# Kernel optimization log

Hardware: AMD Instinct MI355X
Metric: run time of the kernel (lower is better)

The kernel has to match this reference:

```python
import math
import jax, jax.numpy as jnp
import numpy as np

B, T_BI, D_BI = 64, 3000, 128
T_SW, D_SW = 375, 192
T_S1, D_S1 = 188, 192
N_FIRES = 300          # static fire count (target_lengths all = 300 -> beta = 1, ceil(sum)=300)
D_MODEL = 512
SCALE = 4.0            # scale_factor
EPS_LN = 1e-5


def _cif_integrate(h, alpha, thr, n_fires):
    """Vectorized CIF: cumsum + two scatter-adds (matches torch _cif_forward).
    h [B,T,D], alpha [B,T], thr [B,1] -> [B,n_fires,D]."""
    Bq, T, D = h.shape
    a = alpha / thr                       # normalize so boundaries sit at integers
    c = jnp.cumsum(a, axis=1)
    prev = c - a
    kp = jnp.floor(prev)
    kc = jnp.floor(c)
    fired = kc > kp                       # frame crosses a token boundary
    w_hi = jnp.where(fired, (c - kc) * thr, 0.0)          # leftover into new token
    w_lo = jnp.where(fired, (kp + 1.0 - prev) * thr, alpha)  # portion completing old token
    ip = jnp.clip(kp.astype(jnp.int32), 0, n_fires - 1)
    ic = jnp.clip(kc.astype(jnp.int32), 0, n_fires - 1)
    bidx = jnp.broadcast_to(jnp.arange(Bq)[:, None], (Bq, T))
    out = jnp.zeros((Bq, n_fires, D), h.dtype)
    out = out.at[bidx, ip].add(w_lo[..., None] * h)
    out = out.at[bidx, ic].add(w_hi[..., None] * h)
    return out


def _interp(src, t_cont, t_bi):
    """Linear interp of src [B,Ts,D] at continuous fire times t_cont [B,N] (given on the T_bi grid)."""
    Bq, Ts, D = src.shape
    t = t_cont * Ts / t_bi
    lo = jnp.clip(t.astype(jnp.int32), 0, Ts - 2)
    w = (t - lo.astype(t.dtype))[..., None]
    idx_lo = jnp.broadcast_to(lo[..., None], (Bq, t.shape[1], D))
    g_lo = jnp.take_along_axis(src, idx_lo, axis=1)
    g_hi = jnp.take_along_axis(src, idx_lo + 1, axis=1)
    return (1.0 - w) * g_lo + w * g_hi


def _forward(fire_signal, acoustic_src, acoustic_src_s1, conv_w, ln_g, ln_b, wp_w, wp_b,
             film_s0_w, film_s0_b, film_s1_w, film_s1_b, tproj_w, tproj_b,
             aproj_w, aproj_b, bproj_w, bproj_b, target_lengths):
    Bq, T_bi, _ = fire_signal.shape
    # 1) weight predictor: depthwise conv (k=1, no bias) -> LN -> Linear -> sigmoid
    x = fire_signal * conv_w                                   # depthwise 1x1 conv
    mu = jnp.mean(x, axis=-1, keepdims=True)
    var = jnp.var(x, axis=-1, keepdims=True)
    xn = (x - mu) * jax.lax.rsqrt(var + EPS_LN) * ln_g + ln_b
    alpha = SCALE * jax.nn.sigmoid(xn @ wp_w + wp_b)           # [B,T]
    tgt = target_lengths.astype(alpha.dtype)
    qty_loss = jnp.mean(jnp.abs(jnp.sum(alpha, axis=1) - tgt))
    # training-mode alpha normalization (sum alpha_cif == target)
    sum_a = jnp.clip(jnp.sum(alpha, axis=1, keepdims=True), 1e-8)
    alpha_cif = alpha * (tgt[:, None] / sum_a)
    # dynamic threshold beta = sum / ceil(sum)  (== 1 here since targets are integers)
    sum_cif = jnp.sum(alpha_cif, axis=1)
    ceil_sum = jax.lax.stop_gradient(jnp.clip(jnp.ceil(sum_cif), 1.0))
    thr = (sum_cif / ceil_sum)[:, None]                        # [B,1]
    # 2) CIF integration of temporal channel
    acoustic_temporal = _cif_integrate(fire_signal, alpha_cif, thr, N_FIRES)  # [B,N,128]
    # continuous fire times
    cum = jnp.cumsum(alpha_cif, axis=1)
    thresholds = jnp.arange(1, N_FIRES + 1, dtype=alpha.dtype)[None, :] * thr  # [B,N]
    ff = jax.vmap(jnp.searchsorted)(cum, thresholds)
    ff = jnp.minimum(ff, T_bi - 1)
    t_lo = jnp.maximum(ff - 1, 0)
    cum_at = jnp.take_along_axis(cum, t_lo, axis=1)
    a_at = jnp.take_along_axis(alpha_cif, ff, axis=1)
    t_cont = t_lo.astype(alpha.dtype) + (thresholds - cum_at) / jnp.clip(a_at, 1e-8)
    t_cont = jnp.clip(t_cont, 0.0, T_bi - 1)
    # 3) S0 pitch channel: interp + FiLM
    acoustic_pitch = _interp(acoustic_src, t_cont, T_bi)       # [B,N,192]
    film0 = acoustic_temporal @ film_s0_w + film_s0_b
    g0, b0 = jnp.split(film0, 2, axis=-1)
    pitch_mod = g0 * acoustic_pitch + b0
    # 4) project + combine
    embs = (acoustic_temporal @ tproj_w + tproj_b) + (pitch_mod @ aproj_w + aproj_b)
    # S1 beat channel
    acoustic_beat = _interp(acoustic_src_s1, t_cont, T_bi)     # [B,N,192]
    film1 = acoustic_temporal @ film_s1_w + film_s1_b
    g1, b1 = jnp.split(film1, 2, axis=-1)
    beat_mod = g1 * acoustic_beat + b1
    embs = embs + (beat_mod @ bproj_w + bproj_b)
    return embs, alpha, qty_loss


def setup_inputs() -> dict:
    key = jax.random.key(0)
    ks = jax.random.split(key, 14)
    # weight_proj bias init per module: alpha_init = target_fires/encoder_len
    p = min((128.0 / 3000.0) / SCALE, 0.99)
    wp_bias = math.log(p / (1.0 - p))
    f32 = jnp.float32
    return {
        "fire_signal": jax.random.normal(ks[0], (B, T_BI, D_BI), f32),
        "acoustic_src": jax.random.normal(ks[1], (B, T_SW, D_SW), f32),
        "acoustic_src_s1": jax.random.normal(ks[2], (B, T_S1, D_S1), f32),
        "target_lengths": jnp.full((B,), N_FIRES, jnp.int32),
        "conv_w": 1.0 + 0.1 * jax.random.normal(ks[3], (D_BI,), f32),
        "ln_g": jnp.ones((D_BI,), f32),
        "ln_b": jnp.zeros((D_BI,), f32),
        "wp_w": 0.02 * jax.random.normal(ks[4], (D_BI,), f32),
        "wp_b": jnp.asarray(wp_bias, f32),
        "film_s0_w": 0.02 * jax.random.normal(ks[5], (D_BI, 2 * D_SW), f32),
        "film_s0_b": jnp.concatenate([jnp.ones((D_SW,), f32), jnp.zeros((D_SW,), f32)]),
        "film_s1_w": 0.02 * jax.random.normal(ks[6], (D_BI, 2 * D_S1), f32),
        "film_s1_b": jnp.concatenate([jnp.ones((D_S1,), f32), jnp.zeros((D_S1,), f32)]),
        "tproj_w": 0.02 * jax.random.normal(ks[7], (D_BI, D_MODEL), f32),
        "tproj_b": jnp.zeros((D_MODEL,), f32),
        "aproj_w": 0.02 * jax.random.normal(ks[8], (D_SW, D_MODEL), f32),
        "aproj_b": jnp.zeros((D_MODEL,), f32),
        "bproj_w": 0.02 * jax.random.normal(ks[9], (D_S1, D_MODEL), f32),
        "bproj_b": jnp.zeros((D_MODEL,), f32),
    }


def reference(fire_signal, acoustic_src, acoustic_src_s1, target_lengths, conv_w, ln_g, ln_b,
              wp_w, wp_b, film_s0_w, film_s0_b, film_s1_w, film_s1_b, tproj_w, tproj_b,
              aproj_w, aproj_b, bproj_w, bproj_b):
    return _forward(fire_signal, acoustic_src, acoustic_src_s1, conv_w, ln_g, ln_b, wp_w, wp_b,
                    film_s0_w, film_s0_b, film_s1_w, film_s1_b, tproj_w, tproj_b,
                    aproj_w, aproj_b, bproj_w, bproj_b, target_lengths)
```

## Files before the change

kernel.cpp:

```cpp
#include <hip/hip_runtime.h>
#include <math.h>

#define BQ 64
#define TBI 3000
#define DBI 128
#define TSW 375
#define TS1 188
#define DSW 192
#define NF 300
#define DMODEL 512
#define EPSLN 1e-5f

typedef __bf16 bf16x8 __attribute__((ext_vector_type(8)));
typedef float f32x4 __attribute__((ext_vector_type(4)));

__device__ __forceinline__ unsigned short f2bf(float f) {
    unsigned u = __float_as_uint(f);
    unsigned r = (u + 0x7FFFu + ((u >> 16) & 1u)) >> 16;
    return (unsigned short)r;
}

#define ALPHA_BLOCKS 24000

__global__ __launch_bounds__(256) void k_alpha_prep(
    const float* __restrict__ fs, const float* __restrict__ conv_w,
    const float* __restrict__ ln_g, const float* __restrict__ ln_b,
    const float* __restrict__ wp_w, const float* __restrict__ wp_b,
    float* __restrict__ alpha_out,
    const float* __restrict__ f0w, const float* __restrict__ f1w,
    const float* __restrict__ tw, const float* __restrict__ aw, const float* __restrict__ bw,
    const float* __restrict__ f0b, const float* __restrict__ f1b,
    const float* __restrict__ tb, const float* __restrict__ apb, const float* __restrict__ bpb,
    unsigned short* __restrict__ Wg, unsigned short* __restrict__ Wb,
    unsigned short* __restrict__ W2,
    float* __restrict__ gbias, float* __restrict__ bbias, float* __restrict__ bias2,
    float* __restrict__ qtyo)
{
    if (blockIdx.x >= ALPHA_BLOCKS) {
        int pbid = blockIdx.x - ALPHA_BLOCKS;
        if (pbid == 1216) {
            for (int c = threadIdx.x; c < 512; c += 256) {
                if (c < 384) {
                    gbias[c] = c < 192 ? f0b[c] : f1b[c - 192];
                    bbias[c] = c < 192 ? f0b[c + 192] : f1b[c - 192 + 192];
                }
                bias2[c] = tb[c] + apb[c] + bpb[c];
            }
            if (threadIdx.x == 0) qtyo[0] = 0.f;
            return;
        }
        int i = pbid * 256 + threadIdx.x;
        if (i < 49152) {
            int j = i & 7, lane = (i >> 3) & 63, kt = (i >> 9) & 3, nt = i >> 11;
            int k = kt * 32 + (lane >> 4) * 8 + j;
            int n = nt * 16 + (lane & 15);
            float g, b;
            if (n < 192) { g = f0w[k * 384 + n];         b = f0w[k * 384 + n + 192]; }
            else         { g = f1w[k * 384 + (n - 192)]; b = f1w[k * 384 + (n - 192) + 192]; }
            Wg[i] = f2bf(g); Wb[i] = f2bf(b);
        } else {
            int ii = i - 49152;
            int j = ii & 7, lane = (ii >> 3) & 63, kt = (ii >> 9) & 15, nt = ii >> 13;
            int k = kt * 32 + (lane >> 4) * 8 + j;
            int n = nt * 16 + (lane & 15);
            float v;
            if (k < 128)      v = tw[k * 512 + n];
            else if (k < 320) v = aw[(k - 128) * 512 + n];
            else              v = bw[(k - 320) * 512 + n];
            W2[ii] = f2bf(v);
        }
        return;
    }
    int wave = threadIdx.x >> 6, lane = threadIdx.x & 63;
    int l = lane & 31;
    long g = (long)blockIdx.x * 8 + wave * 2 + (lane >> 5);
    const float* row = fs + g * DBI;
    float4 f  = *(const float4*)&row[4 * l];
    float4 cw = *(const float4*)&conv_w[4 * l];
    float4 x; x.x = f.x * cw.x; x.y = f.y * cw.y; x.z = f.z * cw.z; x.w = f.w * cw.w;
    float s = x.x + x.y + x.z + x.w;
    for (int m = 16; m >= 1; m >>= 1) s += __shfl_xor(s, m, 64);
    float mu = s * (1.0f / 128.0f);
    float4 d; d.x = x.x - mu; d.y = x.y - mu; d.z = x.z - mu; d.w = x.w - mu;
    float q = d.x * d.x + d.y * d.y + d.z * d.z + d.w * d.w;
    for (int m = 16; m >= 1; m >>= 1) q += __shfl_xor(q, m, 64);
    float var = q * (1.0f / 128.0f);
    float rs = rsqrtf(var + EPSLN);
    float4 lg = *(const float4*)&ln_g[4 * l];
    float4 lb = *(const float4*)&ln_b[4 * l];
    float4 wp = *(const float4*)&wp_w[4 * l];
    float z = (d.x * rs * lg.x + lb.x) * wp.x + (d.y * rs * lg.y + lb.y) * wp.y
            + (d.z * rs * lg.z + lb.z) * wp.z + (d.w * rs * lg.w + lb.w) * wp.w;
    for (int m = 16; m >= 1; m >>= 1) z += __shfl_xor(z, m, 64);
    z += wp_b[0];
    float a = 4.0f / (1.0f + expf(-z));
    if (l == 0) alpha_out[g] = a;
}

__global__ __launch_bounds__(1024) void k_scan4(
    const float* __restrict__ alpha, const int* __restrict__ tlen,
    float2* __restrict__ params, float* __restrict__ qtyo,
    float2* __restrict__ c2, float* __restrict__ tcont, int* __restrict__ ffout)
{
    __shared__ float2 sc[TBI];
    __shared__ float2 part[2][1024];
    __shared__ double wpart[16];
    int b = blockIdx.x, tid = threadIdx.x;
    int wv = tid >> 6, ln = tid & 63;
    const float* ar = alpha + (long)b * TBI;
    double s = 0.0;
    for (int t = tid; t < TBI; t += 1024) s += (double)ar[t];
    for (int m = 32; m >= 1; m >>= 1) s += __shfl_xor(s, m, 64);
    if (ln == 0) wpart[wv] = s;
    __syncthreads();
    if (wv == 0) {
        double d = (ln < 16) ? wpart[ln] : 0.0;
        for (int m = 8; m >= 1; m >>= 1) d += __shfl_xor(d, m, 64);
        if (ln == 0) wpart[0] = d;
    }
    __syncthreads();
    double sum_a = wpart[0];
    __syncthreads();
    double tgt = (double)tlen[b];
    double sa = sum_a < 1e-8 ? 1e-8 : sum_a;
    float r = (float)(tgt / sa);
    double s2 = 0.0;
    for (int t = tid; t < TBI; t += 1024) s2 += (double)(ar[t] * r);
    for (int m = 32; m >= 1; m >>= 1) s2 += __shfl_xor(s2, m, 64);
    if (ln == 0) wpart[wv] = s2;
    __syncthreads();
    if (wv == 0) {
        double d = (ln < 16) ? wpart[ln] : 0.0;
        for (int m = 8; m >= 1; m >>= 1) d += __shfl_xor(d, m, 64);
        if (ln == 0) wpart[0] = d;
    }
    __syncthreads();
    float sum_cif = (float)wpart[0];
    float cs = ceilf(sum_cif); if (cs < 1.0f) cs = 1.0f;
    float thr = sum_cif / cs;
    float rthr = 1.0f / thr;
    if (tid == 0) {
        params[b] = make_float2(r, thr);
        atomicAdd(qtyo, (float)fabs(sum_a - tgt) * (1.0f / (float)BQ));
    }
    int base = tid * 3;
    float2 run = make_float2(0.f, 0.f);
    if (base < TBI) {
        for (int j = 0; j < 3; ++j) {
            int t = base + j;
            float ac = ar[t] * r;
            run.x += ac * rthr; run.y += ac;
            sc[t] = run;
        }
    }
    part[0][tid] = (base < TBI) ? run : make_float2(0.f, 0.f);
    __syncthreads();
    int srcb = 0;
    for (int d = 1; d < 1024; d <<= 1) {
        float2 v = part[srcb][tid];
        if (tid >= d) { float2 u = part[srcb][tid - d]; v.x += u.x; v.y += u.y; }
        part[srcb ^ 1][tid] = v;
        srcb ^= 1;
        __syncthreads();
    }
    if (base < TBI && tid > 0) {
        float2 off = part[srcb][tid - 1];
        for (int j = 0; j < 3; ++j) { sc[base + j].x += off.x; sc[base + j].y += off.y; }
    }
    __syncthreads();
    for (int t = tid; t < TBI; t += 1024) {
        float ac = ar[t] * r;
        c2[(long)b * TBI + t] = make_float2(sc[t].x, ac);
    }
    if (tid < NF) {
        float v = (float)(tid + 1) * thr;
        int lo = 0, hi = TBI;
        while (lo < hi) { int mid = (lo + hi) >> 1; if (sc[mid].y < v) lo = mid + 1; else hi = mid; }
        int ff = lo; if (ff > TBI - 1) ff = TBI - 1;
        ffout[b * NF + tid] = ff;
        int tl = ff - 1; if (tl < 0) tl = 0;
        float cum_at = sc[tl].y;
        float a_at = ar[ff] * r;
        if (a_at < 1e-8f) a_at = 1e-8f;
        float tc = (float)tl + (v - cum_at) / a_at;
        tc = fminf(fmaxf(tc, 0.0f), (float)(TBI - 1));
        tcont[b * NF + tid] = tc;
    }
}

__global__ __launch_bounds__(256) void k_cif5(
    const float* __restrict__ fs, const float2* __restrict__ c2,
    const int* __restrict__ ffA, const float2* __restrict__ params,
    unsigned short* __restrict__ at)
{
    int wid = threadIdx.x >> 6, lane = threadIdx.x & 63;
    int wg = blockIdx.x * 4 + wid;
    int b = wg / NF, j = wg - b * NF;
    const int* ffb = ffA + b * NF;
    int s = (j == 0) ? 0 : ffb[j - 1];
    int e = (j == NF - 1) ? (TBI - 1) : ffb[j];
    float thr = params[b].y;
    float rthr = 1.0f / thr;
    const float2* cb = c2 + (long)b * TBI;
    const float* fb = fs + (long)b * TBI * DBI;
    float a0 = 0.f, a1 = 0.f;
    #define CIF_BODY(T) do { \
        float2 v = cb[T]; \
        float2 h = *(const float2*)&fb[(long)(T) * DBI + 2 * lane]; \
        float c = v.x, ac = v.y; \
        float av = ac * rthr; \
        float prev = c - av; \
        float kp = floorf(prev), kc = floorf(c); \
        bool fired = kc > kp; \
        float w_lo = fired ? (kp + 1.0f - prev) * thr : ac; \
        float w_hi = fired ? (c - kc) * thr : 0.0f; \
        int ip = (int)kp; if (ip > NF - 1) ip = NF - 1; if (ip < 0) ip = 0; \
        int ic = (int)kc; if (ic > NF - 1) ic = NF - 1; if (ic < 0) ic = 0; \
        if (ip == j) { a0 += w_lo * h.x; a1 += w_lo * h.y; } \
        if (fired && ic == j) { a0 += w_hi * h.x; a1 += w_hi * h.y; } \
    } while (0)
    int t = s;
    for (; t + 1 <= e; t += 2) { CIF_BODY(t); CIF_BODY(t + 1); }
    if (t <= e) CIF_BODY(t);
    #undef CIF_BODY
    unsigned short* ab = at + (long)b * NF * DBI;
    *(unsigned*)&ab[j * DBI + 2 * lane] = (unsigned)f2bf(a0) | ((unsigned)f2bf(a1) << 16);
}

#define EROWS 32
__global__ __launch_bounds__(512, 4) void k_emb8(
    const unsigned short* __restrict__ atb, const float* __restrict__ tcont,
    const float* __restrict__ src0, const float* __restrict__ src1,
    const unsigned short* __restrict__ Wg, const unsigned short* __restrict__ Wb,
    const unsigned short* __restrict__ W2,
    const float* __restrict__ gbias, const float* __restrict__ bbias,
    const float* __restrict__ bias2, float* __restrict__ embs)
{
    __shared__ __align__(16) unsigned short X[EROWS][520];
    __shared__ float s_w0[EROWS], s_w1[EROWS];
    __shared__ int s_lo0[EROWS], s_lo1[EROWS], s_b[EROWS];
    int tid = threadIdx.x;
    int wave = tid >> 6, lane = tid & 63;
    long r0 = (long)blockIdx.x * EROWS;
    {
        int r = tid >> 4, k8 = (tid & 15) * 8;
        *(uint4*)&X[r][k8] = *(const uint4*)&atb[(r0 + r) * DBI + k8];
    }
    if (tid < EROWS) {
        long g = r0 + tid;
        s_b[tid] = (int)(g / NF);
        float tc = tcont[g];
        float t0 = tc * ((float)TSW / 3000.0f);
        int lo0 = (int)t0; if (lo0 > TSW - 2) lo0 = TSW - 2; if (lo0 < 0) lo0 = 0;
        s_lo0[tid] = lo0; s_w0[tid] = t0 - (float)lo0;
        float t1 = tc * ((float)TS1 / 3000.0f);
        int lo1 = (int)t1; if (lo1 > TS1 - 2) lo1 = TS1 - 2; if (lo1 < 0) lo1 = 0;
        s_lo1[tid] = lo1; s_w1[tid] = t1 - (float)lo1;
    }
    __syncthreads();
    int mrow = lane & 15, quad = lane >> 4;
    float v0[3][2][4], v1[3][2][4], wgt[3][2][4];
    float gbv[3], bbv_[3];
    #pragma unroll
    for (int i = 0; i < 3; ++i) {
        int nt = wave + 8 * i;
        int c = nt * 16 + mrow;
        bool sel = c >= DSW;
        int cc = sel ? c - DSW : c;
        const float* S = sel ? src1 : src0;
        int Ts = sel ? TS1 : TSW;
        gbv[i] = gbias[c]; bbv_[i] = bbias[c];
        #pragma unroll
        for (int m = 0; m < 2; ++m) {
            #pragma unroll
            for (int q = 0; q < 4; ++q) {
                int r = 16 * m + quad * 4 + q;
                int bb = s_b[r];
                int lo = sel ? s_lo1[r] : s_lo0[r];
                float w = sel ? s_w1[r] : s_w0[r];
                const float* Sp = S + ((long)bb * Ts + lo) * DSW + cc;
                v0[i][m][q] = Sp[0];
                v1[i][m][q] = Sp[DSW];
                wgt[i][m][q] = w;
            }
        }
    }
    #pragma unroll
    for (int i = 0; i < 3; ++i) {
        int nt = wave + 8 * i;
        f32x4 ag0 = {0,0,0,0}, ab0 = {0,0,0,0}, ag1 = {0,0,0,0}, ab1 = {0,0,0,0};
        #pragma unroll
        for (int kt = 0; kt < 4; ++kt) {
            bf16x8 a0 = *(const bf16x8*)&X[mrow][kt * 32 + quad * 8];
            bf16x8 a1 = *(const bf16x8*)&X[mrow + 16][kt * 32 + quad * 8];
            bf16x8 bg = *(const bf16x8*)&Wg[(((nt * 4 + kt) * 64) + lane) * 8];
            bf16x8 bb = *(const bf16x8*)&Wb[(((nt * 4 + kt) * 64) + lane) * 8];
            ag0 = __builtin_amdgcn_mfma_f32_16x16x32_bf16(a0, bg, ag0, 0, 0, 0);
            ab0 = __builtin_amdgcn_mfma_f32_16x16x32_bf16(a0, bb, ab0, 0, 0, 0);
            ag1 = __builtin_amdgcn_mfma_f32_16x16x32_bf16(a1, bg, ag1, 0, 0, 0);
            ab1 = __builtin_amdgcn_mfma_f32_16x16x32_bf16(a1, bb, ab1, 0, 0, 0);
        }
        int c = nt * 16 + mrow;
        float gb = gbv[i], bbv = bbv_[i];
        #pragma unroll
        for (int q = 0; q < 4; ++q) {
            {
                int r = quad * 4 + q;
                float w = wgt[i][0][q];
                float pv = (1.0f - w) * v0[i][0][q] + w * v1[i][0][q];
                X[r][128 + c] = f2bf((ag0[q] + gb) * pv + (ab0[q] + bbv));
            }
            {
                int r = quad * 4 + q + 16;
                float w = wgt[i][1][q];
                float pv = (1.0f - w) * v0[i][1][q] + w * v1[i][1][q];
                X[r][128 + c] = f2bf((ag1[q] + gb) * pv + (ab1[q] + bbv));
            }
        }
    }
    __syncthreads();
    f32x4 acc[2][4];
    #pragma unroll
    for (int h = 0; h < 2; ++h)
        #pragma unroll
        for (int n = 0; n < 4; ++n) acc[h][n] = (f32x4){0, 0, 0, 0};
    for (int kt = 0; kt < 16; ++kt) {
        bf16x8 a0 = *(const bf16x8*)&X[mrow][kt * 32 + quad * 8];
        bf16x8 a1 = *(const bf16x8*)&X[mrow + 16][kt * 32 + quad * 8];
        #pragma unroll
        for (int n = 0; n < 4; ++n) {
            int nt = wave * 4 + n;
            bf16x8 bfv = *(const bf16x8*)&W2[((nt * 16 + kt) * 64 + lane) * 8];
            acc[0][n] = __builtin_amdgcn_mfma_f32_16x16x32_bf16(a0, bfv, acc[0][n], 0, 0, 0);
            acc[1][n] = __builtin_amdgcn_mfma_f32_16x16x32_bf16(a1, bfv, acc[1][n], 0, 0, 0);
        }
    }
    #pragma unroll
    for (int n = 0; n < 4; ++n) {
        int cbase = (wave * 4 + n) * 16 + mrow;
        float bv = bias2[cbase];
        #pragma unroll
        for (int q = 0; q < 4; ++q) {
            embs[(r0 + quad * 4 + q) * DMODEL + cbase] = acc[0][n][q] + bv;
            embs[(r0 + 16 + quad * 4 + q) * DMODEL + cbase] = acc[1][n][q] + bv;
        }
    }
}

extern "C" void kernel_launch(void* const* d_in, const int* in_sizes, int n_in,
                              void* d_out, int out_size, void* d_ws, size_t ws_size,
                              hipStream_t stream)
{
    const float* fs     = (const float*)d_in[0];
    const float* src0   = (const float*)d_in[1];
    const float* src1   = (const float*)d_in[2];
    const int*   tlen   = (const int*)d_in[3];
    const float* conv_w = (const float*)d_in[4];
    const float* ln_g   = (const float*)d_in[5];
    const float* ln_b   = (const float*)d_in[6];
    const float* wp_w   = (const float*)d_in[7];
    const float* wp_b   = (const float*)d_in[8];
    const float* f0w    = (const float*)d_in[9];
    const float* f0b    = (const float*)d_in[10];
    const float* f1w    = (const float*)d_in[11];
    const float* f1b    = (const float*)d_in[12];
    const float* tw     = (const float*)d_in[13];
    const float* tb     = (const float*)d_in[14];
    const float* aw     = (const float*)d_in[15];
    const float* apb    = (const float*)d_in[16];
    const float* bw     = (const float*)d_in[17];
    const float* bpb    = (const float*)d_in[18];

    float* embs  = (float*)d_out;
    float* alpha = embs + (long)BQ * NF * DMODEL;
    float* qtyo  = alpha + (long)BQ * TBI;

    char* ws = (char*)d_ws;
    size_t off = 0;
    unsigned short* at = (unsigned short*)(ws + off); off += 4915200;
    float2* c2     = (float2*)(ws + off); off += 1536000;
    float*  tcont  = (float*)(ws + off);  off += 76800;
    int*    ffA    = (int*)(ws + off);    off += 76800;
    float2* params = (float2*)(ws + off); off += 512;
    unsigned short* Wg = (unsigned short*)(ws + off); off += 98304;
    unsigned short* Wb = (unsigned short*)(ws + off); off += 98304;
    unsigned short* W2 = (unsigned short*)(ws + off); off += 524288;
    float* gbias = (float*)(ws + off); off += 1536;
    float* bbias = (float*)(ws + off); off += 1536;
    float* bias2 = (float*)(ws + off); off += 2048;

    k_alpha_prep<<<ALPHA_BLOCKS + 1217, 256, 0, stream>>>(
        fs, conv_w, ln_g, ln_b, wp_w, wp_b, alpha,
        f0w, f1w, tw, aw, bw, f0b, f1b, tb, apb, bpb,
        Wg, Wb, W2, gbias, bbias, bias2, qtyo);
    k_scan4<<<BQ, 1024, 0, stream>>>(alpha, tlen, params, qtyo, c2, tcont, ffA);
    k_cif5<<<(BQ * NF) / 4, 256, 0, stream>>>(fs, c2, ffA, params, at);
    k_emb8<<<(BQ * NF) / EROWS, 512, 0, stream>>>(at, tcont, src0, src1,
                                                  Wg, Wb, W2, gbias, bbias, bias2, embs);
}
```

Before: 264.6 us.

## Halve embedding kernel block size and load interp sources inline after MFMA

The embedding kernel now uses 256 threads (4 waves) per 32-row block instead of 512. Each wave handles twice as many FiLM and output column tiles (6 FiLM tiles, 8 output tiles). The interpolation source values are no longer prefetched into a large register array before the MFMAs; they are loaded inline in the epilogue. This cuts register pressure and raises per-wave W2 reuse of the A fragments, but exposes gather latency after the MFMAs and lowers parallelism per block.

```diff
diff --git a/kernel.cpp b/kernel.cpp
--- a/kernel.cpp
+++ b/kernel.cpp
@@ -228,7 +228,7 @@
 }
 
 #define EROWS 32
-__global__ __launch_bounds__(512, 4) void k_emb8(
+__global__ __launch_bounds__(256, 3) void k_emb9(
     const unsigned short* __restrict__ atb, const float* __restrict__ tcont,
     const float* __restrict__ src0, const float* __restrict__ src1,
     const unsigned short* __restrict__ Wg, const unsigned short* __restrict__ Wb,
@@ -242,8 +242,8 @@
     int tid = threadIdx.x;
     int wave = tid >> 6, lane = tid & 63;
     long r0 = (long)blockIdx.x * EROWS;
-    {
-        int r = tid >> 4, k8 = (tid & 15) * 8;
+    for (int idx = tid; idx < 512; idx += 256) {
+        int r = idx >> 4, k8 = (idx & 15) * 8;
         *(uint4*)&X[r][k8] = *(const uint4*)&atb[(r0 + r) * DBI + k8];
     }
     if (tid < EROWS) {
@@ -259,35 +259,8 @@
     }
     __syncthreads();
     int mrow = lane & 15, quad = lane >> 4;
-    float v0[3][2][4], v1[3][2][4], wgt[3][2][4];
-    float gbv[3], bbv_[3];
-    #pragma unroll
-    for (int i = 0; i < 3; ++i) {
-        int nt = wave + 8 * i;
-        int c = nt * 16 + mrow;
-        bool sel = c >= DSW;
-        int cc = sel ? c - DSW : c;
-        const float* S = sel ? src1 : src0;
-        int Ts = sel ? TS1 : TSW;
-        gbv[i] = gbias[c]; bbv_[i] = bbias[c];
-        #pragma unroll
-        for (int m = 0; m < 2; ++m) {
-            #pragma unroll
-            for (int q = 0; q < 4; ++q) {
-                int r = 16 * m + quad * 4 + q;
-                int bb = s_b[r];
-                int lo = sel ? s_lo1[r] : s_lo0[r];
-                float w = sel ? s_w1[r] : s_w0[r];
-                const float* Sp = S + ((long)bb * Ts + lo) * DSW + cc;
-                v0[i][m][q] = Sp[0];
-                v1[i][m][q] = Sp[DSW];
-                wgt[i][m][q] = w;
-            }
-        }
-    }
-    #pragma unroll
-    for (int i = 0; i < 3; ++i) {
-        int nt = wave + 8 * i;
+    for (int i = 0; i < 6; ++i) {
+        int nt = wave + 4 * i;
         f32x4 ag0 = {0,0,0,0}, ab0 = {0,0,0,0}, ag1 = {0,0,0,0}, ab1 = {0,0,0,0};
         #pragma unroll
         for (int kt = 0; kt < 4; ++kt) {
@@ -301,43 +274,53 @@
             ab1 = __builtin_amdgcn_mfma_f32_16x16x32_bf16(a1, bb, ab1, 0, 0, 0);
         }
         int c = nt * 16 + mrow;
-        float gb = gbv[i], bbv = bbv_[i];
+        bool sel = c >= DSW;
+        int cc = sel ? c - DSW : c;
+        const float* S = sel ? src1 : src0;
+        int Ts = sel ? TS1 : TSW;
+        float gb = gbias[c], bbv = bbias[c];
         #pragma unroll
         for (int q = 0; q < 4; ++q) {
             {
                 int r = quad * 4 + q;
-                float w = wgt[i][0][q];
-                float pv = (1.0f - w) * v0[i][0][q] + w * v1[i][0][q];
+                int b = s_b[r];
+                int lo = sel ? s_lo1[r] : s_lo0[r];
+                float w = sel ? s_w1[r] : s_w0[r];
+                const float* Sp = S + ((long)b * Ts + lo) * DSW + cc;
+                float pv = (1.0f - w) * Sp[0] + w * Sp[DSW];
                 X[r][128 + c] = f2bf((ag0[q] + gb) * pv + (ab0[q] + bbv));
             }
             {
                 int r = quad * 4 + q + 16;
-                float w = wgt[i][1][q];
-                float pv = (1.0f - w) * v0[i][1][q] + w * v1[i][1][q];
+                int b = s_b[r];
+                int lo = sel ? s_lo1[r] : s_lo0[r];
+                float w = sel ? s_w1[r] : s_w0[r];
+                const float* Sp = S + ((long)b * Ts + lo) * DSW + cc;
+                float pv = (1.0f - w) * Sp[0] + w * Sp[DSW];
                 X[r][128 + c] = f2bf((ag1[q] + gb) * pv + (ab1[q] + bbv));
             }
         }
     }
     __syncthreads();
-    f32x4 acc[2][4];
+    f32x4 acc[2][8];
     #pragma unroll
     for (int h = 0; h < 2; ++h)
         #pragma unroll
-        for (int n = 0; n < 4; ++n) acc[h][n] = (f32x4){0, 0, 0, 0};
+        for (int n = 0; n < 8; ++n) acc[h][n] = (f32x4){0, 0, 0, 0};
     for (int kt = 0; kt < 16; ++kt) {
         bf16x8 a0 = *(const bf16x8*)&X[mrow][kt * 32 + quad * 8];
         bf16x8 a1 = *(const bf16x8*)&X[mrow + 16][kt * 32 + quad * 8];
         #pragma unroll
-        for (int n = 0; n < 4; ++n) {
-            int nt = wave * 4 + n;
+        for (int n = 0; n < 8; ++n) {
+            int nt = wave * 8 + n;
             bf16x8 bfv = *(const bf16x8*)&W2[((nt * 16 + kt) * 64 + lane) * 8];
             acc[0][n] = __builtin_amdgcn_mfma_f32_16x16x32_bf16(a0, bfv, acc[0][n], 0, 0, 0);
             acc[1][n] = __builtin_amdgcn_mfma_f32_16x16x32_bf16(a1, bfv, acc[1][n], 0, 0, 0);
         }
     }
     #pragma unroll
-    for (int n = 0; n < 4; ++n) {
-        int cbase = (wave * 4 + n) * 16 + mrow;
+    for (int n = 0; n < 8; ++n) {
+        int cbase = (wave * 8 + n) * 16 + mrow;
         float bv = bias2[cbase];
         #pragma unroll
         for (int q = 0; q < 4; ++q) {
@@ -395,6 +378,6 @@
         Wg, Wb, W2, gbias, bbias, bias2, qtyo);
     k_scan4<<<BQ, 1024, 0, stream>>>(alpha, tlen, params, qtyo, c2, tcont, ffA);
     k_cif5<<<(BQ * NF) / 4, 256, 0, stream>>>(fs, c2, ffA, params, at);
-    k_emb8<<<(BQ * NF) / EROWS, 512, 0, stream>>>(at, tcont, src0, src1,
+    k_emb9<<<(BQ * NF) / EROWS, 256, 0, stream>>>(at, tcont, src0, src1,
                                                   Wg, Wb, W2, gbias, bbias, bias2, embs);
 }
```

New measurement: 262.6 us. No clear change (-0.8%).
